# Optimization experiments

Measured on AMD Instinct MI355X. Metric: run time of the kernel, lower is better.

The kernel has to match this reference:

```python
import jax, jax.numpy as jnp
import numpy as np

E = 1024
M = 6
GH = 256
FR = 16  # FiLM bottleneck r = max(16, E//64)


def setup_inputs() -> dict:
    key = jax.random.key(0)
    ks = jax.random.split(key, 32)
    n = lambda k, shape, std=0.02: jax.random.normal(k, shape, dtype=jnp.float32) * std
    inp = {
        "x": jax.random.normal(ks[0], (4, 2048, E), dtype=jnp.float32),
        # gate MLP E->GH->M
        "gw1": n(ks[1], (E, GH)), "gb1": jnp.zeros((GH,), jnp.float32),
        "gw2": n(ks[2], (GH, M)), "gb2": jnp.zeros((M,), jnp.float32),
        "ebias": jnp.zeros((M,), jnp.float32),
        "pm_alpha": jnp.float32(0.5),
        # expert 0: DoubleMLP E->2E->E
        "dfc_w": n(ks[3], (E, 2 * E)), "dfc_b": jnp.zeros((2 * E,), jnp.float32),
        "dproj_w": n(ks[4], (2 * E, E)), "dproj_b": jnp.zeros((E,), jnp.float32),
        # expert 1: SingleMLP E->E->E
        "sfc_w": n(ks[5], (E, E)), "sfc_b": jnp.zeros((E,), jnp.float32),
        "sproj_w": n(ks[6], (E, E)), "sproj_b": jnp.zeros((E,), jnp.float32),
        # expert 2: rank-2 perceptron
        "p2_w": n(ks[7], (2, E)), "p2_v": n(ks[8], (2, E)),
        "p2_alpha": jnp.ones((2,), jnp.float32), "p2_b": jnp.zeros((2,), jnp.float32),
        "p2_bias": jnp.zeros((E,), jnp.float32),
        # expert 3: rank-4 perceptron
        "p4_w": n(ks[9], (4, E)), "p4_v": n(ks[10], (4, E)),
        "p4_alpha": jnp.ones((4,), jnp.float32), "p4_b": jnp.zeros((4,), jnp.float32),
        "p4_bias": jnp.zeros((E,), jnp.float32),
        # expert 4: ReGLU1D
        "rg_u": n(ks[11], (E,)), "rg_a": jnp.ones((E,), jnp.float32),
        "rg_b": jnp.zeros((1,), jnp.float32), "rg_bias": jnp.zeros((E,), jnp.float32),
        # expert 5: FiLM E->FR->2E
        "fl_dw": n(ks[12], (E, FR)), "fl_db": jnp.zeros((FR,), jnp.float32),
        "fl_uw": n(ks[13], (FR, 2 * E)), "fl_ub": jnp.zeros((2 * E,), jnp.float32),
    }
    return inp


def _gelu(x):
    return jax.nn.gelu(x, approximate=False)  # torch nn.GELU default (erf)


def _rank_n(x, w, v, alpha, b, biasvec):
    # y = biasvec + sum_i alpha_i * gelu(<w_i,x> + b_i) * v_i
    s = jnp.einsum("bse,ne->bsn", x, w) + b
    g = _gelu(s)
    return jnp.einsum("bsn,ne->bse", alpha * g, v) + biasvec


def reference(x, gw1, gb1, gw2, gb2, ebias, pm_alpha,
              dfc_w, dfc_b, dproj_w, dproj_b,
              sfc_w, sfc_b, sproj_w, sproj_b,
              p2_w, p2_v, p2_alpha, p2_b, p2_bias,
              p4_w, p4_v, p4_alpha, p4_b, p4_bias,
              rg_u, rg_a, rg_b, rg_bias,
              fl_dw, fl_db, fl_uw, fl_ub):
    # gate logits [B,S,M]; tau=1.0
    gl = _gelu(x @ gw1 + gb1) @ gw2 + gb2 + ebias
    pi = jax.nn.softmax(gl, axis=-1)
    # top_k=1 sparse weights: mask to top-1 then renormalize
    _, topi = jax.lax.top_k(pi, 1)
    mask = jax.nn.one_hot(topi[..., 0], M, dtype=pi.dtype)
    w = pi * mask
    w = w / (jnp.sum(w, axis=-1, keepdims=True) + 1e-9)

    # experts (dropout = identity in eval)
    o0 = _gelu(x @ dfc_w + dfc_b) @ dproj_w + dproj_b            # DoubleMLP
    o1 = _gelu(x @ sfc_w + sfc_b) @ sproj_w + sproj_b            # SingleMLP
    o2 = _rank_n(x, p2_w, p2_v, p2_alpha, p2_b, p2_bias)          # perc2
    o3 = _rank_n(x, p4_w, p4_v, p4_alpha, p4_b, p4_bias)          # perc4
    s = x @ rg_u + rg_b[0]                                        # ReGLU1D
    o4 = jax.nn.sigmoid(s)[..., None] * (x * rg_a) + rg_bias
    t = _gelu(x @ fl_dw + fl_db)                                  # FiLM
    gb = t @ fl_uw + fl_ub
    gamma, beta = jnp.split(gb, 2, axis=-1)
    o5 = gamma * x + beta

    all_out = jnp.stack([o0, o1, o2, o3, o4, o5], axis=-1)        # [B,S,E,M]
    mixed = jnp.sum(all_out * w[..., None, :], axis=-1)
    return pm_alpha * mixed
```

## Files before the change

kernel.cpp:

```cpp
#include <hip/hip_runtime.h>
#include <math.h>


#define E 1024
#define GH 256
#define NEXP 6
#define NTOK 8192
#define NCH 24

typedef __attribute__((ext_vector_type(8))) short bf16x8;
typedef __attribute__((ext_vector_type(4))) float f32x4;

__device__ __forceinline__ float gelu_erf(float v) {
    return 0.5f * v * (1.0f + erff(v * 0.70710678118654752440f));
}

__device__ __forceinline__ unsigned short f2bf(float f) {
    union { float f; unsigned u; } c; c.f = f;
    unsigned u = c.u;
    u += 0x7fffu + ((u >> 16) & 1u);
    return (unsigned short)(u >> 16);
}

__device__ __forceinline__ float bf2f(unsigned short h) {
    union { unsigned u; float f; } c; c.u = ((unsigned)h) << 16;
    return c.f;
}

__device__ __forceinline__ int ldso(int row, int q) {
    return row * 32 + ((q ^ ((row >> 1) & 3)) << 3);
}

__device__ __forceinline__ void glds16(const void* g, void* l) {
    __builtin_amdgcn_global_load_lds(
        (const __attribute__((address_space(1))) void*)g,
        (__attribute__((address_space(3))) void*)l, 16, 0, 0);
}

__global__ __launch_bounds__(256)
void prep_kernel(const float* __restrict__ x, unsigned short* __restrict__ xh,
                 unsigned short* __restrict__ xl,
                 const float* __restrict__ gw1, unsigned short* __restrict__ w1cat,
                 const float* __restrict__ p2_w, const float* __restrict__ p4_w,
                 const float* __restrict__ rg_u, const float* __restrict__ fl_dw,
                 unsigned short* __restrict__ w1cheap,
                 const float* __restrict__ dfc_w, unsigned short* __restrict__ dfc_wt,
                 const float* __restrict__ dproj_w, unsigned short* __restrict__ dpj_wt,
                 const float* __restrict__ sfc_w, unsigned short* __restrict__ sfc_wt,
                 const float* __restrict__ sproj_w, unsigned short* __restrict__ spj_wt) {
    __shared__ float tile[32][33];
    const int tid = threadIdx.x;
    const int tx = tid & 31, ty = tid >> 5;
    int b = blockIdx.x;
    if (b < 2048) {
        const int n4 = NTOK * E / 4;
        for (int i = b * 256 + tid; i < n4; i += 2048 * 256) {
            float4 v = reinterpret_cast<const float4*>(x)[i];
            ushort4 h, l;
            h.x = f2bf(v.x); l.x = f2bf(v.x - bf2f(h.x));
            h.y = f2bf(v.y); l.y = f2bf(v.y - bf2f(h.y));
            h.z = f2bf(v.z); l.z = f2bf(v.z - bf2f(h.z));
            h.w = f2bf(v.w); l.w = f2bf(v.w - bf2f(h.w));
            reinterpret_cast<ushort4*>(xh)[i] = h;
            reinterpret_cast<ushort4*>(xl)[i] = l;
        }
        return;
    }
    b -= 2048;
    if (b < 256) {
        const int c0 = (b & 7) * 32, r0 = (b >> 3) * 32;
#pragma unroll
        for (int i = 0; i < 4; ++i)
            tile[ty + i * 8][tx] = gw1[(size_t)(r0 + ty + i * 8) * GH + c0 + tx];
        __syncthreads();
#pragma unroll
        for (int i = 0; i < 4; ++i) {
            float v = tile[tx][ty + i * 8];
            unsigned short h = f2bf(v);
            size_t row = (size_t)(c0 + ty + i * 8) * 2048;
            w1cat[row + r0 + tx] = h;
            w1cat[row + 1024 + r0 + tx] = f2bf(v - bf2f(h));
        }
        return;
    }
    b -= 256;
    if (b < 64) {
        const int r = b;
        const int k4 = tid * 4;
        float4 v = {0.f, 0.f, 0.f, 0.f};
        if (r < 2)       v = *reinterpret_cast<const float4*>(&p2_w[r * E + k4]);
        else if (r < 6)  v = *reinterpret_cast<const float4*>(&p4_w[(r - 2) * E + k4]);
        else if (r == 6) v = *reinterpret_cast<const float4*>(&rg_u[k4]);
        else if (r < 23) {
            const int j = r - 7;
            v.x = fl_dw[(k4 + 0) * 16 + j];
            v.y = fl_dw[(k4 + 1) * 16 + j];
            v.z = fl_dw[(k4 + 2) * 16 + j];
            v.w = fl_dw[(k4 + 3) * 16 + j];
        }
        ushort4 h, l;
        h.x = f2bf(v.x); l.x = f2bf(v.x - bf2f(h.x));
        h.y = f2bf(v.y); l.y = f2bf(v.y - bf2f(h.y));
        h.z = f2bf(v.z); l.z = f2bf(v.z - bf2f(h.z));
        h.w = f2bf(v.w); l.w = f2bf(v.w - bf2f(h.w));
        *reinterpret_cast<ushort4*>(&w1cheap[r * 2048 + k4]) = h;
        *reinterpret_cast<ushort4*>(&w1cheap[r * 2048 + 1024 + k4]) = l;
        return;
    }
    b -= 64;
    const float* src; unsigned short* dst; int R, C, nbx;
    if (b < 2048)      { src = dfc_w;   dst = dfc_wt; R = 1024; C = 2048; nbx = 64; }
    else if (b < 4096) { src = dproj_w; dst = dpj_wt; R = 2048; C = 1024; nbx = 32; b -= 2048; }
    else if (b < 5120) { src = sfc_w;   dst = sfc_wt; R = 1024; C = 1024; nbx = 32; b -= 4096; }
    else               { src = sproj_w; dst = spj_wt; R = 1024; C = 1024; nbx = 32; b -= 5120; }
    const int c0 = (b % nbx) * 32, r0 = (b / nbx) * 32;
#pragma unroll
    for (int i = 0; i < 4; ++i)
        tile[ty + i * 8][tx] = src[(size_t)(r0 + ty + i * 8) * C + c0 + tx];
    __syncthreads();
#pragma unroll
    for (int i = 0; i < 4; ++i)
        dst[(size_t)(c0 + ty + i * 8) * R + r0 + tx] = f2bf(tile[tx][ty + i * 8]);
}

__global__ __launch_bounds__(256)
void gate_partial_kernel(const unsigned short* __restrict__ xh,
                         const unsigned short* __restrict__ xl,
                         const unsigned short* __restrict__ w1cat,
                         const unsigned short* __restrict__ w1cheap,
                         float* __restrict__ hp,
                         float* __restrict__ cdot) {
    __shared__ __align__(16) unsigned short As[2][128 * 64];
    __shared__ __align__(16) unsigned short Bs[2][128 * 64];
    const int tid = threadIdx.x;
    const int bid = blockIdx.x;
    const int xcd = bid & 7, slot = bid >> 3;
    const int nx = slot & 1;
    const int strip = xcd * 32 + (slot >> 1);
    const int m = strip >> 2, c2 = strip & 3;
    const int z = c2 & 1, h = c2 >> 1;
    const int t0 = m * 128, n0 = nx * 128;
    const unsigned short* A = z ? xl : xh;
    float* hpz = hp + (size_t)c2 * ((size_t)NTOK * GH);
    float* cd  = cdot + (size_t)c2 * ((size_t)NTOK * NCH);

    const int lane = tid & 63, wv = tid >> 6;
    const int wr = wv >> 1, wc = wv & 1;
    const int lm = lane & 15, q = lane >> 4;
    const int r0 = tid >> 2, gsl = tid & 3;
    const int g = gsl ^ ((r0 >> 1) & 3);
    const int lbase = wv * 512;

    const unsigned short* pa0 = A + (size_t)(t0 + r0) * E + g * 8;
    const unsigned short* pa1 = A + (size_t)(t0 + 64 + r0) * E + g * 8;
    const unsigned short* pb0 = w1cat + (size_t)(n0 + r0) * 2048 + h * 1024 + g * 8;
    const unsigned short* pb1 = w1cat + (size_t)(n0 + 64 + r0) * 2048 + h * 1024 + g * 8;
    const unsigned short* pcw = w1cheap + (size_t)(nx * 16 + lm) * 2048 + h * 1024 + q * 8;

    f32x4 acc[4][4];
#pragma unroll
    for (int s = 0; s < 4; ++s)
#pragma unroll
        for (int t = 0; t < 4; ++t) acc[s][t] = (f32x4){0.f, 0.f, 0.f, 0.f};
    f32x4 accC[2];
    accC[0] = (f32x4){0.f, 0.f, 0.f, 0.f};
    accC[1] = (f32x4){0.f, 0.f, 0.f, 0.f};

    glds16(pa0, &As[0][lbase]);
    glds16(pa1, &As[0][2048 + lbase]);
    glds16(pa0 + 32, &As[0][4096 + lbase]);
    glds16(pa1 + 32, &As[0][4096 + 2048 + lbase]);
    glds16(pb0, &Bs[0][lbase]);
    glds16(pb1, &Bs[0][2048 + lbase]);
    glds16(pb0 + 32, &Bs[0][4096 + lbase]);
    glds16(pb1 + 32, &Bs[0][4096 + 2048 + lbase]);
    bf16x8 cf0 = *(const bf16x8*)pcw;
    bf16x8 cf1 = *(const bf16x8*)(pcw + 32);

    int cur = 0;
    for (int k0 = 0;; k0 += 64) {
        __syncthreads();
        const int kn = k0 + 64;
        bf16x8 cf0n, cf1n;
        if (kn < 1024) {
            glds16(pa0 + kn, &As[cur ^ 1][lbase]);
            glds16(pa1 + kn, &As[cur ^ 1][2048 + lbase]);
            glds16(pa0 + kn + 32, &As[cur ^ 1][4096 + lbase]);
            glds16(pa1 + kn + 32, &As[cur ^ 1][4096 + 2048 + lbase]);
            glds16(pb0 + kn, &Bs[cur ^ 1][lbase]);
            glds16(pb1 + kn, &Bs[cur ^ 1][2048 + lbase]);
            glds16(pb0 + kn + 32, &Bs[cur ^ 1][4096 + lbase]);
            glds16(pb1 + kn + 32, &Bs[cur ^ 1][4096 + 2048 + lbase]);
            cf0n = *(const bf16x8*)(pcw + kn);
            cf1n = *(const bf16x8*)(pcw + kn + 32);
        }
#pragma unroll
        for (int sub = 0; sub < 2; ++sub) {
            const int off = sub * 4096;
            bf16x8 af[4], bfr[4];
#pragma unroll
            for (int s = 0; s < 4; ++s) af[s] = *(const bf16x8*)&As[cur][off + ldso(wr * 64 + s * 16 + lm, q)];
#pragma unroll
            for (int t = 0; t < 4; ++t) bfr[t] = *(const bf16x8*)&Bs[cur][off + ldso(wc * 64 + t * 16 + lm, q)];
#pragma unroll
            for (int s = 0; s < 4; ++s)
#pragma unroll
                for (int t = 0; t < 4; ++t)
                    acc[s][t] = __builtin_amdgcn_mfma_f32_16x16x32_bf16(af[s], bfr[t], acc[s][t], 0, 0, 0);
            bf16x8 cf = sub ? cf1 : cf0;
            bf16x8 ac0 = wc ? af[2] : af[0];
            bf16x8 ac1 = wc ? af[3] : af[1];
            accC[0] = __builtin_amdgcn_mfma_f32_16x16x32_bf16(ac0, cf, accC[0], 0, 0, 0);
            accC[1] = __builtin_amdgcn_mfma_f32_16x16x32_bf16(ac1, cf, accC[1], 0, 0, 0);
        }
        if (kn >= 1024) break;
        cf0 = cf0n; cf1 = cf1n; cur ^= 1;
    }
#pragma unroll
    for (int s = 0; s < 4; ++s)
#pragma unroll
        for (int t = 0; t < 4; ++t)
#pragma unroll
            for (int rg = 0; rg < 4; ++rg) {
                int rl = wr * 64 + s * 16 + q * 4 + rg;
                int c  = wc * 64 + t * 16 + lm;
                hpz[(size_t)(t0 + rl) * GH + n0 + c] = acc[s][t][rg];
            }
    const int cc = nx * 16 + lm;
    if (cc < NCH) {
#pragma unroll
        for (int i = 0; i < 2; ++i)
#pragma unroll
            for (int rg = 0; rg < 4; ++rg) {
                int rl = wr * 64 + wc * 32 + i * 16 + q * 4 + rg;
                cd[(size_t)(t0 + rl) * NCH + cc] = accC[i][rg];
            }
    }
}

__global__ __launch_bounds__(256)
void gate_finalize_kernel(const float* __restrict__ hp,
                          const float* __restrict__ gb1, const float* __restrict__ gw2,
                          const float* __restrict__ gb2, const float* __restrict__ ebias,
                          const float* __restrict__ pm_alpha,
                          const float* __restrict__ cdot,
                          const float* __restrict__ p2_alpha, const float* __restrict__ p2_b,
                          const float* __restrict__ p4_alpha, const float* __restrict__ p4_b,
                          const float* __restrict__ rg_b, const float* __restrict__ fl_db,
                          float* __restrict__ scale, int* __restrict__ counts,
                          int* __restrict__ tlist, int* __restrict__ eid,
                          float* __restrict__ gvec) {
    __shared__ float hs[32][264];
    __shared__ float g2s[GH * NEXP];
    __shared__ int tokexp[32];
    const int tid = threadIdx.x;
    const int t0 = blockIdx.x * 32;
    const size_t HPS = (size_t)NTOK * GH;
    for (int i = tid; i < GH * NEXP; i += 256) g2s[i] = gw2[i];
#pragma unroll
    for (int i = 0; i < 8; ++i) {
        int f4 = i * 256 + tid;
        int row = f4 >> 6, c4 = (f4 & 63) * 4;
        size_t base = (size_t)(t0 + row) * GH + c4;
        float4 a = *reinterpret_cast<const float4*>(&hp[base]);
        float4 b = *reinterpret_cast<const float4*>(&hp[HPS + base]);
        float4 c = *reinterpret_cast<const float4*>(&hp[2 * HPS + base]);
        float4 d = *reinterpret_cast<const float4*>(&hp[3 * HPS + base]);
        float4 o;
        o.x = gelu_erf(a.x + b.x + c.x + d.x + gb1[c4 + 0]);
        o.y = gelu_erf(a.y + b.y + c.y + d.y + gb1[c4 + 1]);
        o.z = gelu_erf(a.z + b.z + c.z + d.z + gb1[c4 + 2]);
        o.w = gelu_erf(a.w + b.w + c.w + d.w + gb1[c4 + 3]);
        *reinterpret_cast<float4*>(&hs[row][c4]) = o;
    }
    __syncthreads();
    const int t = tid >> 3, j = tid & 7;
    float p[NEXP] = {0.f, 0.f, 0.f, 0.f, 0.f, 0.f};
#pragma unroll 8
    for (int kk = 0; kk < 32; ++kk) {
        int k = j + kk * 8;
        float hv = hs[t][k];
        const float* gr = &g2s[k * NEXP];
#pragma unroll
        for (int m = 0; m < NEXP; ++m) p[m] += hv * gr[m];
    }
#pragma unroll
    for (int m = 0; m < NEXP; ++m) {
        p[m] += __shfl_xor(p[m], 4, 64);
        p[m] += __shfl_xor(p[m], 2, 64);
        p[m] += __shfl_xor(p[m], 1, 64);
    }
    if (j == 0) {
        float L[NEXP];
#pragma unroll
        for (int m = 0; m < NEXP; ++m) L[m] = p[m] + gb2[m] + ebias[m];
        float mx = L[0]; int am = 0;
#pragma unroll
        for (int m = 1; m < NEXP; ++m) { if (L[m] > mx) { mx = L[m]; am = m; } }
        float S = 0.f;
#pragma unroll
        for (int m = 0; m < NEXP; ++m) S += expf(L[m] - mx);
        float pt = 1.f / S;
        scale[t0 + t] = pm_alpha[0] * (pt / (pt + 1e-9f));
        eid[t0 + t] = am;
        tokexp[t] = am;
    }
    __syncthreads();
    if (tid < NEXP) {
        const int e = tid;
        int cnt = 0;
#pragma unroll
        for (int i = 0; i < 32; ++i) cnt += (tokexp[i] == e);
        if (cnt) {
            int base = atomicAdd(&counts[e], cnt);
            int pos = 0;
#pragma unroll
            for (int i = 0; i < 32; ++i)
                if (tokexp[i] == e) tlist[e * NTOK + base + (pos++)] = t0 + i;
        }
    }
    const size_t CDS = (size_t)NTOK * NCH;
    for (int i = tid; i < 32 * NCH; i += 256) {
        const int tt = i / NCH, slot = i - tt * NCH;
        const int tok = t0 + tt;
        size_t idx = (size_t)tok * NCH + slot;
        float s = cdot[idx] + cdot[CDS + idx] + cdot[2 * CDS + idx] + cdot[3 * CDS + idx];
        float val;
        if (slot < 2)       val = p2_alpha[slot] * gelu_erf(s + p2_b[slot]);
        else if (slot < 6)  val = p4_alpha[slot - 2] * gelu_erf(s + p4_b[slot - 2]);
        else if (slot == 6) val = 1.f / (1.f + expf(-(s + rg_b[0])));
        else if (slot < 23) val = gelu_erf(s + fl_db[slot - 7]);
        else                val = 0.f;
        gvec[(size_t)tok * NCH + slot] = val;
    }
}

#define STAGEAB(t, jb)                                            \
    do {                                                          \
        glds16(pa + (t) * 64,      &As[jb][lbase]);               \
        glds16(pa + (t) * 64 + 32, &As[jb][2048 + lbase]);        \
        glds16(pb + (t) * 64,      &Bs[jb][lbase]);               \
        glds16(pb + (t) * 64 + 32, &Bs[jb][2048 + lbase]);        \
    } while (0)

__global__ __launch_bounds__(256)
void moe_gemm1_kernel(const unsigned short* __restrict__ xh,
                      const unsigned short* __restrict__ B0, const unsigned short* __restrict__ B1,
                      const float* __restrict__ bias0, const float* __restrict__ bias1,
                      const int* __restrict__ counts, const int* __restrict__ tlist,
                      unsigned short* __restrict__ H0, unsigned short* __restrict__ H1) {
    __shared__ __align__(16) unsigned short As[3][64 * 64];
    __shared__ __align__(16) unsigned short Bs[3][64 * 64];
    __shared__ int toks[64];
    const int tid = threadIdx.x;
    const int bid = blockIdx.x;
    const int xcd = bid & 7, slot = bid >> 3;
    const int nx = slot & 31;
    const int strip = xcd + 8 * (slot >> 5);
    const int z = strip & 1;
    const int N = z ? 1024 : 2048;
    const int cnt = counts[z];
    const int i0 = (strip >> 1) * 64;
    const int n0 = nx * 64;
    if (i0 >= cnt || n0 >= N) return;
    const unsigned short* Bz = z ? B1 : B0;
    const float* bias = z ? bias1 : bias0;

    if (tid < 64) toks[tid] = tlist[z * NTOK + min(i0 + tid, cnt - 1)];
    __syncthreads();

    const int lane = tid & 63, wv = tid >> 6;
    const int wm = (wv & 1) * 32, wn = (wv >> 1) * 32;
    const int lm = lane & 15, q = lane >> 4;
    const int r0 = tid >> 2, gsl = tid & 3;
    const int g = gsl ^ ((r0 >> 1) & 3);
    const int lbase = wv * 512;

    const unsigned short* pa = xh + (size_t)toks[r0] * E + g * 8;
    const unsigned short* pb = Bz + (size_t)(n0 + r0) * E + g * 8;

    f32x4 acc[2][2];
#pragma unroll
    for (int s = 0; s < 2; ++s)
#pragma unroll
        for (int t = 0; t < 2; ++t) acc[s][t] = (f32x4){0.f, 0.f, 0.f, 0.f};

    STAGEAB(0, 0); STAGEAB(1, 1); STAGEAB(2, 2);

    const int nt = E / 64;
    for (int i = 0; i < nt; ++i) {
        const int ahead = nt - 1 - i;
        if (ahead >= 2)      asm volatile("s_waitcnt vmcnt(8)" ::: "memory");
        else if (ahead == 1) asm volatile("s_waitcnt vmcnt(4)" ::: "memory");
        else                 asm volatile("s_waitcnt vmcnt(0)" ::: "memory");
        asm volatile("s_barrier" ::: "memory");
        const int jb = i % 3;
#pragma unroll
        for (int sub = 0; sub < 2; ++sub) {
            const int off = sub * 2048;
            bf16x8 af[2], bfr[2];
#pragma unroll
            for (int s = 0; s < 2; ++s) af[s] = *(const bf16x8*)&As[jb][off + ldso(wm + s * 16 + lm, q)];
#pragma unroll
            for (int t = 0; t < 2; ++t) bfr[t] = *(const bf16x8*)&Bs[jb][off + ldso(wn + t * 16 + lm, q)];
#pragma unroll
            for (int s = 0; s < 2; ++s)
#pragma unroll
                for (int t = 0; t < 2; ++t)
                    acc[s][t] = __builtin_amdgcn_mfma_f32_16x16x32_bf16(af[s], bfr[t], acc[s][t], 0, 0, 0);
        }
        asm volatile("s_barrier" ::: "memory");
        if (i + 3 < nt) STAGEAB(i + 3, jb);
    }
    unsigned short* Hz = z ? H1 : H0;
#pragma unroll
    for (int s = 0; s < 2; ++s)
#pragma unroll
        for (int t = 0; t < 2; ++t)
#pragma unroll
            for (int rg = 0; rg < 4; ++rg) {
                int rl = wm + s * 16 + q * 4 + rg;
                int gc = n0 + wn + t * 16 + lm;
                float v = acc[s][t][rg] + bias[gc];
                Hz[(size_t)(i0 + rl) * N + gc] = f2bf(gelu_erf(v));
            }
}

__global__ __launch_bounds__(256)
void moe_gemm2_kernel(const unsigned short* __restrict__ h1, const unsigned short* __restrict__ h2,
                      const unsigned short* __restrict__ dpj, const unsigned short* __restrict__ spj,
                      const float* __restrict__ dproj_b, const float* __restrict__ sproj_b,
                      const int* __restrict__ counts, const int* __restrict__ tlist,
                      const float* __restrict__ scale,
                      float* __restrict__ out) {
    __shared__ __align__(16) unsigned short As[3][64 * 64];
    __shared__ __align__(16) unsigned short Bs[3][64 * 64];
    __shared__ int toks[64];
    const int tid = threadIdx.x;
    const int bb = blockIdx.x;
    const int lane = tid & 63;

    const int xcd = bb & 7, slot = bb >> 3;
    const int nx = slot & 15;
    const int strip = xcd + 8 * (slot >> 4);
    const int z = strip & 1;
    const int i0 = (strip >> 1) * 64;
    const int n0 = nx * 64;
    const int K = z ? 1024 : 2048;
    const int cnt = counts[z];
    if (i0 >= cnt) return;
    const int rows = min(64, cnt - i0);
    const unsigned short* Az = z ? h2 : h1;
    const unsigned short* Bz = z ? spj : dpj;
    const float* bias = z ? sproj_b : dproj_b;

    if (tid < 64) toks[tid] = tlist[z * NTOK + min(i0 + tid, cnt - 1)];
    __syncthreads();

    const int wv = tid >> 6;
    const int wm = (wv & 1) * 32, wn = (wv >> 1) * 32;
    const int lm = lane & 15, q = lane >> 4;
    const int r0 = tid >> 2, gsl = tid & 3;
    const int g = gsl ^ ((r0 >> 1) & 3);
    const int lbase = wv * 512;

    const unsigned short* pa = Az + (size_t)(i0 + r0) * K + g * 8;
    const unsigned short* pb = Bz + (size_t)(n0 + r0) * K + g * 8;

    f32x4 acc[2][2];
#pragma unroll
    for (int s = 0; s < 2; ++s)
#pragma unroll
        for (int t = 0; t < 2; ++t) acc[s][t] = (f32x4){0.f, 0.f, 0.f, 0.f};

    STAGEAB(0, 0); STAGEAB(1, 1); STAGEAB(2, 2);

    const int nt = K / 64;
    for (int i = 0; i < nt; ++i) {
        const int ahead = nt - 1 - i;
        if (ahead >= 2)      asm volatile("s_waitcnt vmcnt(8)" ::: "memory");
        else if (ahead == 1) asm volatile("s_waitcnt vmcnt(4)" ::: "memory");
        else                 asm volatile("s_waitcnt vmcnt(0)" ::: "memory");
        asm volatile("s_barrier" ::: "memory");
        const int jb = i % 3;
#pragma unroll
        for (int sub = 0; sub < 2; ++sub) {
            const int off = sub * 2048;
            bf16x8 af[2], bfr[2];
#pragma unroll
            for (int s = 0; s < 2; ++s) af[s] = *(const bf16x8*)&As[jb][off + ldso(wm + s * 16 + lm, q)];
#pragma unroll
            for (int t = 0; t < 2; ++t) bfr[t] = *(const bf16x8*)&Bs[jb][off + ldso(wn + t * 16 + lm, q)];
#pragma unroll
            for (int s = 0; s < 2; ++s)
#pragma unroll
                for (int t = 0; t < 2; ++t)
                    acc[s][t] = __builtin_amdgcn_mfma_f32_16x16x32_bf16(af[s], bfr[t], acc[s][t], 0, 0, 0);
        }
        asm volatile("s_barrier" ::: "memory");
        if (i + 3 < nt) STAGEAB(i + 3, jb);
    }
#pragma unroll
    for (int s = 0; s < 2; ++s)
#pragma unroll
        for (int t = 0; t < 2; ++t)
#pragma unroll
            for (int rg = 0; rg < 4; ++rg) {
                int rl = wm + s * 16 + q * 4 + rg;
                if (rl < rows) {
                    int gc = n0 + wn + t * 16 + lm;
                    int tok = toks[rl];
                    out[(size_t)tok * E + gc] = scale[tok] * (acc[s][t][rg] + bias[gc]);
                }
            }
}

__global__ __launch_bounds__(256)
void cheap_kernel(const int* __restrict__ counts, const int* __restrict__ tlist,
                  const float* __restrict__ scale, const float* __restrict__ x,
                  const float* __restrict__ gvec,
                  const float* __restrict__ p2_v, const float* __restrict__ p2_bias,
                  const float* __restrict__ p4_v, const float* __restrict__ p4_bias,
                  const float* __restrict__ rg_a, const float* __restrict__ rg_bias,
                  const float* __restrict__ fl_uw, const float* __restrict__ fl_ub,
                  float* __restrict__ out) {
    __shared__ int stoks[8];
    __shared__ float ssc[8];
    __shared__ float sgv[8][17];
    const int tid = threadIdx.x;
    const int k4 = tid * 4;
    for (int s = blockIdx.x; s < 4096; s += 2048) {
        const int e = 2 + (s & 3);
        const int ti = s >> 2;
        const int cnt = counts[e];
        const int i0 = ti * 8;
        if (i0 >= cnt) continue;
        const int nt = min(8, cnt - i0);
        __syncthreads();
        if (tid < 128) {
            const int tt = tid >> 4, sl = tid & 15;
            const int tk = tlist[e * NTOK + min(i0 + tt, cnt - 1)];
            if (sl == 0) { stoks[tt] = tk; ssc[tt] = scale[tk]; }
            const int base = (e == 2) ? 0 : (e == 3) ? 2 : (e == 4) ? 6 : 7;
            const int ng   = (e == 2) ? 2 : (e == 3) ? 4 : (e == 4) ? 1 : 16;
            if (sl < ng) sgv[tt][sl] = gvec[(size_t)tk * NCH + base + sl];
        }
        __syncthreads();
        if (e == 2) {
            const float4 b0 = *reinterpret_cast<const float4*>(&p2_bias[k4]);
            const float4 v0 = *reinterpret_cast<const float4*>(&p2_v[k4]);
            const float4 v1 = *reinterpret_cast<const float4*>(&p2_v[E + k4]);
#pragma unroll
            for (int tt = 0; tt < 8; ++tt) {
                if (tt < nt) {
                    const float g0 = sgv[tt][0], g1 = sgv[tt][1], sc = ssc[tt];
                    float4 o;
                    o.x = (b0.x + g0 * v0.x + g1 * v1.x) * sc;
                    o.y = (b0.y + g0 * v0.y + g1 * v1.y) * sc;
                    o.z = (b0.z + g0 * v0.z + g1 * v1.z) * sc;
                    o.w = (b0.w + g0 * v0.w + g1 * v1.w) * sc;
                    *reinterpret_cast<float4*>(&out[(size_t)stoks[tt] * E + k4]) = o;
                }
            }
        } else if (e == 3) {
            const float4 b0 = *reinterpret_cast<const float4*>(&p4_bias[k4]);
            float4 vv[4];
#pragma unroll
            for (int j = 0; j < 4; ++j)
                vv[j] = *reinterpret_cast<const float4*>(&p4_v[j * E + k4]);
#pragma unroll
            for (int tt = 0; tt < 8; ++tt) {
                if (tt < nt) {
                    float4 o = b0;
#pragma unroll
                    for (int j = 0; j < 4; ++j) {
                        const float gj = sgv[tt][j];
                        o.x += gj * vv[j].x; o.y += gj * vv[j].y;
                        o.z += gj * vv[j].z; o.w += gj * vv[j].w;
                    }
                    const float sc = ssc[tt];
                    o.x *= sc; o.y *= sc; o.z *= sc; o.w *= sc;
                    *reinterpret_cast<float4*>(&out[(size_t)stoks[tt] * E + k4]) = o;
                }
            }
        } else if (e == 4) {
            const float4 av = *reinterpret_cast<const float4*>(&rg_a[k4]);
            const float4 bv = *reinterpret_cast<const float4*>(&rg_bias[k4]);
#pragma unroll
            for (int tt = 0; tt < 8; ++tt) {
                if (tt < nt) {
                    const float sg = sgv[tt][0], sc = ssc[tt];
                    const float4 xv = *reinterpret_cast<const float4*>(&x[(size_t)stoks[tt] * E + k4]);
                    float4 o;
                    o.x = (sg * xv.x * av.x + bv.x) * sc;
                    o.y = (sg * xv.y * av.y + bv.y) * sc;
                    o.z = (sg * xv.z * av.z + bv.z) * sc;
                    o.w = (sg * xv.w * av.w + bv.w) * sc;
                    *reinterpret_cast<float4*>(&out[(size_t)stoks[tt] * E + k4]) = o;
                }
            }
        } else {
            float4 ga[8], be[8];
            const float4 g0 = *reinterpret_cast<const float4*>(&fl_ub[k4]);
            const float4 b0 = *reinterpret_cast<const float4*>(&fl_ub[E + k4]);
#pragma unroll
            for (int tt = 0; tt < 8; ++tt) { ga[tt] = g0; be[tt] = b0; }
#pragma unroll
            for (int j = 0; j < 16; ++j) {
                const float4 ug = *reinterpret_cast<const float4*>(&fl_uw[(size_t)j * 2 * E + k4]);
                const float4 ub = *reinterpret_cast<const float4*>(&fl_uw[(size_t)j * 2 * E + E + k4]);
#pragma unroll
                for (int tt = 0; tt < 8; ++tt) {
                    const float tj = sgv[tt][j];
                    ga[tt].x += tj * ug.x; ga[tt].y += tj * ug.y;
                    ga[tt].z += tj * ug.z; ga[tt].w += tj * ug.w;
                    be[tt].x += tj * ub.x; be[tt].y += tj * ub.y;
                    be[tt].z += tj * ub.z; be[tt].w += tj * ub.w;
                }
            }
#pragma unroll
            for (int tt = 0; tt < 8; ++tt) {
                if (tt < nt) {
                    const float sc = ssc[tt];
                    const float4 xv = *reinterpret_cast<const float4*>(&x[(size_t)stoks[tt] * E + k4]);
                    float4 o;
                    o.x = (ga[tt].x * xv.x + be[tt].x) * sc;
                    o.y = (ga[tt].y * xv.y + be[tt].y) * sc;
                    o.z = (ga[tt].z * xv.z + be[tt].z) * sc;
                    o.w = (ga[tt].w * xv.w + be[tt].w) * sc;
                    *reinterpret_cast<float4*>(&out[(size_t)stoks[tt] * E + k4]) = o;
                }
            }
        }
    }
}

extern "C" void kernel_launch(void* const* d_in, const int* in_sizes, int n_in,
                              void* d_out, int out_size, void* d_ws, size_t ws_size,
                              hipStream_t stream) {
    const float* x        = (const float*)d_in[0];
    const float* gw1      = (const float*)d_in[1];
    const float* gb1      = (const float*)d_in[2];
    const float* gw2      = (const float*)d_in[3];
    const float* gb2      = (const float*)d_in[4];
    const float* ebias    = (const float*)d_in[5];
    const float* pm_alpha = (const float*)d_in[6];
    const float* dfc_w    = (const float*)d_in[7];
    const float* dfc_b    = (const float*)d_in[8];
    const float* dproj_w  = (const float*)d_in[9];
    const float* dproj_b  = (const float*)d_in[10];
    const float* sfc_w    = (const float*)d_in[11];
    const float* sfc_b    = (const float*)d_in[12];
    const float* sproj_w  = (const float*)d_in[13];
    const float* sproj_b  = (const float*)d_in[14];
    const float* p2_w     = (const float*)d_in[15];
    const float* p2_v     = (const float*)d_in[16];
    const float* p2_alpha = (const float*)d_in[17];
    const float* p2_b     = (const float*)d_in[18];
    const float* p2_bias  = (const float*)d_in[19];
    const float* p4_w     = (const float*)d_in[20];
    const float* p4_v     = (const float*)d_in[21];
    const float* p4_alpha = (const float*)d_in[22];
    const float* p4_b     = (const float*)d_in[23];
    const float* p4_bias  = (const float*)d_in[24];
    const float* rg_u     = (const float*)d_in[25];
    const float* rg_a     = (const float*)d_in[26];
    const float* rg_b     = (const float*)d_in[27];
    const float* rg_bias  = (const float*)d_in[28];
    const float* fl_dw    = (const float*)d_in[29];
    const float* fl_db    = (const float*)d_in[30];
    const float* fl_uw    = (const float*)d_in[31];
    const float* fl_ub    = (const float*)d_in[32];
    float* out = (float*)d_out;

    char* ws = (char*)d_ws;
    size_t off = 0;
    int*            counts = (int*)(ws + off);            off += 256;
    float*          scale  = (float*)(ws + off);          off += (size_t)NTOK * 4;
    int*            tlist  = (int*)(ws + off);            off += (size_t)NEXP * NTOK * 4;
    int*            eid    = (int*)(ws + off);            off += (size_t)NTOK * 4;
    float*          gvec   = (float*)(ws + off);          off += (size_t)NTOK * NCH * 4;
    float*          cdot   = (float*)(ws + off);          off += (size_t)4 * NTOK * NCH * 4;
    unsigned short* w1cheap= (unsigned short*)(ws + off); off += (size_t)64 * 2048 * 2;
    unsigned short* w1cat  = (unsigned short*)(ws + off); off += (size_t)GH * 2048 * 2;
    unsigned short* dfc_wt = (unsigned short*)(ws + off); off += (size_t)2048 * 1024 * 2;
    unsigned short* dpj_wt = (unsigned short*)(ws + off); off += (size_t)1024 * 2048 * 2;
    unsigned short* sfc_wt = (unsigned short*)(ws + off); off += (size_t)1024 * 1024 * 2;
    unsigned short* spj_wt = (unsigned short*)(ws + off); off += (size_t)1024 * 1024 * 2;
    unsigned short* x_hi   = (unsigned short*)(ws + off); off += (size_t)NTOK * E * 2;
    char* U = ws + off;
    unsigned short* x_lo = (unsigned short*)U;
    unsigned short* h1   = (unsigned short*)U;
    unsigned short* h2   = (unsigned short*)(U + (size_t)16 * 1024 * 1024);
    float* hp = out;

    hipMemsetAsync(counts, 0, 256, stream);
    prep_kernel<<<8512, 256, 0, stream>>>(x, x_hi, x_lo, gw1, w1cat,
                                          p2_w, p4_w, rg_u, fl_dw, w1cheap,
                                          dfc_w, dfc_wt, dproj_w, dpj_wt,
                                          sfc_w, sfc_wt, sproj_w, spj_wt);
    gate_partial_kernel<<<512, 256, 0, stream>>>(
        x_hi, x_lo, w1cat, w1cheap, hp, cdot);
    gate_finalize_kernel<<<NTOK / 32, 256, 0, stream>>>(
        hp, gb1, gw2, gb2, ebias, pm_alpha, cdot,
        p2_alpha, p2_b, p4_alpha, p4_b, rg_b, fl_db,
        scale, counts, tlist, eid, gvec);
    moe_gemm1_kernel<<<2048, 256, 0, stream>>>(
        x_hi, dfc_wt, sfc_wt, dfc_b, sfc_b, counts, tlist, h1, h2);
    moe_gemm2_kernel<<<1024, 256, 0, stream>>>(
        h1, h2, dpj_wt, spj_wt, dproj_b, sproj_b, counts, tlist, scale, out);
    cheap_kernel<<<2048, 256, 0, stream>>>(
        counts, tlist, scale, x, gvec,
        p2_v, p2_bias, p4_v, p4_bias,
        rg_a, rg_bias, fl_uw, fl_ub, out);
    (void)in_sizes; (void)n_in; (void)out_size; (void)ws_size;
}
```

Baseline: 283.6 us.

## Fold cheap experts into dense MFMA tiles appended to the gemm1 launch

Removes cheap_kernel and expresses the four cheap experts (two low-rank perceptrons, ReGLU and FiLM) as a small K=32 matmul. Each token gets a coefficient row (split into bf16 hi/lo halves) against packed additive and multiplicative bf16 weight tables, and the result is out = scale*(M*x + A). These tiles run as 2048 extra blocks in the moe_gemm1 launch, which removes a kernel launch and the per-expert scalar loops and lets the work overlap with the big GEMM. In exchange every token's output is computed and written densely, with zeros for tokens routed to the MLP experts until gemm2 overwrites them. The expert weight vectors are now rounded to bf16, which adds some precision risk.

```diff
diff --git a/kernel.cpp b/kernel.cpp
--- a/kernel.cpp
+++ b/kernel.cpp
@@ -44,6 +44,11 @@
                  const float* __restrict__ p2_w, const float* __restrict__ p4_w,
                  const float* __restrict__ rg_u, const float* __restrict__ fl_dw,
                  unsigned short* __restrict__ w1cheap,
+                 const float* __restrict__ p2_bias, const float* __restrict__ p2_v,
+                 const float* __restrict__ p4_bias, const float* __restrict__ p4_v,
+                 const float* __restrict__ rg_a, const float* __restrict__ rg_bias,
+                 const float* __restrict__ fl_uw, const float* __restrict__ fl_ub,
+                 unsigned short* __restrict__ bta, unsigned short* __restrict__ btm,
                  const float* __restrict__ dfc_w, unsigned short* __restrict__ dfc_wt,
                  const float* __restrict__ dproj_w, unsigned short* __restrict__ dpj_wt,
                  const float* __restrict__ sfc_w, unsigned short* __restrict__ sfc_wt,
@@ -108,6 +113,34 @@
         return;
     }
     b -= 64;
+    if (b < 4) {
+        const int n = b * 256 + tid;
+        float av[32], mv[32];
+#pragma unroll
+        for (int r = 0; r < 32; ++r) { av[r] = 0.f; mv[r] = 0.f; }
+        av[0] = p2_bias[n];
+        av[1] = p2_v[n]; av[2] = p2_v[E + n];
+        av[3] = p4_bias[n];
+#pragma unroll
+        for (int j = 0; j < 4; ++j) av[4 + j] = p4_v[j * E + n];
+        av[8] = rg_bias[n];
+        mv[9] = rg_a[n];
+        av[10] = fl_ub[E + n];
+        mv[10] = fl_ub[n];
+#pragma unroll
+        for (int j = 0; j < 16; ++j) {
+            av[11 + j] = fl_uw[(size_t)j * 2 * E + E + n];
+            mv[11 + j] = fl_uw[(size_t)j * 2 * E + n];
+        }
+#pragma unroll
+        for (int r = 0; r < 32; ++r) {
+            unsigned short ha = f2bf(av[r]), hm = f2bf(mv[r]);
+            bta[n * 64 + r] = ha; bta[n * 64 + 32 + r] = ha;
+            btm[n * 64 + r] = hm; btm[n * 64 + 32 + r] = hm;
+        }
+        return;
+    }
+    b -= 4;
     const float* src; unsigned short* dst; int R, C, nbx;
     if (b < 2048)      { src = dfc_w;   dst = dfc_wt; R = 1024; C = 2048; nbx = 64; }
     else if (b < 4096) { src = dproj_w; dst = dpj_wt; R = 2048; C = 1024; nbx = 32; b -= 2048; }
@@ -248,8 +281,8 @@
                           const float* __restrict__ p4_alpha, const float* __restrict__ p4_b,
                           const float* __restrict__ rg_b, const float* __restrict__ fl_db,
                           float* __restrict__ scale, int* __restrict__ counts,
-                          int* __restrict__ tlist, int* __restrict__ eid,
-                          float* __restrict__ gvec) {
+                          int* __restrict__ tlist,
+                          unsigned short* __restrict__ Cm) {
     __shared__ float hs[32][264];
     __shared__ float g2s[GH * NEXP];
     __shared__ int tokexp[32];
@@ -302,7 +335,6 @@
         for (int m = 0; m < NEXP; ++m) S += expf(L[m] - mx);
         float pt = 1.f / S;
         scale[t0 + t] = pm_alpha[0] * (pt / (pt + 1e-9f));
-        eid[t0 + t] = am;
         tokexp[t] = am;
     }
     __syncthreads();
@@ -320,18 +352,31 @@
         }
     }
     const size_t CDS = (size_t)NTOK * NCH;
-    for (int i = tid; i < 32 * NCH; i += 256) {
-        const int tt = i / NCH, slot = i - tt * NCH;
+    for (int i = tid; i < 32 * 32; i += 256) {
+        const int tt = i >> 5, r = i & 31;
         const int tok = t0 + tt;
-        size_t idx = (size_t)tok * NCH + slot;
-        float s = cdot[idx] + cdot[CDS + idx] + cdot[2 * CDS + idx] + cdot[3 * CDS + idx];
-        float val;
-        if (slot < 2)       val = p2_alpha[slot] * gelu_erf(s + p2_b[slot]);
-        else if (slot < 6)  val = p4_alpha[slot - 2] * gelu_erf(s + p4_b[slot - 2]);
-        else if (slot == 6) val = 1.f / (1.f + expf(-(s + rg_b[0])));
-        else if (slot < 23) val = gelu_erf(s + fl_db[slot - 7]);
-        else                val = 0.f;
-        gvec[(size_t)tok * NCH + slot] = val;
+        const int e = tokexp[tt];
+        float c = 0.f;
+        int slot = -1;
+        if (r == 0)       { if (e == 2) c = 1.f; }
+        else if (r <= 2)  { if (e == 2) slot = r - 1; }
+        else if (r == 3)  { if (e == 3) c = 1.f; }
+        else if (r <= 7)  { if (e == 3) slot = r - 2; }
+        else if (r == 8)  { if (e == 4) c = 1.f; }
+        else if (r == 9)  { if (e == 4) slot = 6; }
+        else if (r == 10) { if (e == 5) c = 1.f; }
+        else if (r <= 26) { if (e == 5) slot = r - 4; }
+        if (slot >= 0) {
+            size_t idx = (size_t)tok * NCH + slot;
+            float s = cdot[idx] + cdot[CDS + idx] + cdot[2 * CDS + idx] + cdot[3 * CDS + idx];
+            if (slot < 2)       c = p2_alpha[slot] * gelu_erf(s + p2_b[slot]);
+            else if (slot < 6)  c = p4_alpha[slot - 2] * gelu_erf(s + p4_b[slot - 2]);
+            else if (slot == 6) c = 1.f / (1.f + expf(-(s + rg_b[0])));
+            else                c = gelu_erf(s + fl_db[slot - 7]);
+        }
+        unsigned short hi = f2bf(c);
+        Cm[(size_t)tok * 64 + r] = hi;
+        Cm[(size_t)tok * 64 + 32 + r] = f2bf(c - bf2f(hi));
     }
 }
 
@@ -348,12 +393,87 @@
                       const unsigned short* __restrict__ B0, const unsigned short* __restrict__ B1,
                       const float* __restrict__ bias0, const float* __restrict__ bias1,
                       const int* __restrict__ counts, const int* __restrict__ tlist,
-                      unsigned short* __restrict__ H0, unsigned short* __restrict__ H1) {
+                      unsigned short* __restrict__ H0, unsigned short* __restrict__ H1,
+                      const unsigned short* __restrict__ Cm,
+                      const unsigned short* __restrict__ bta, const unsigned short* __restrict__ btm,
+                      const float* __restrict__ x, const float* __restrict__ scale,
+                      float* __restrict__ out) {
     __shared__ __align__(16) unsigned short As[3][64 * 64];
     __shared__ __align__(16) unsigned short Bs[3][64 * 64];
     __shared__ int toks[64];
     const int tid = threadIdx.x;
     const int bid = blockIdx.x;
+    const int lane = tid & 63, wv = tid >> 6;
+    const int wm = (wv & 1) * 32, wn = (wv >> 1) * 32;
+    const int lm = lane & 15, q = lane >> 4;
+    const int r0 = tid >> 2, gsl = tid & 3;
+    const int g = gsl ^ ((r0 >> 1) & 3);
+    const int lbase = wv * 512;
+
+    if (bid >= 2048) {
+        const int cg = bid - 2048;
+        const int xcd = cg & 7, s = cg >> 3;
+        const int nx = s & 15;
+        const int mt = xcd + 8 * (s >> 4);
+        const int t0 = mt * 64, n0 = nx * 64;
+        unsigned short* Ct = &As[0][0];
+        unsigned short* Ba = &As[1][0];
+        unsigned short* Bm = &As[2][0];
+
+        const unsigned short* pc = Cm + (size_t)(t0 + r0) * 64 + g * 8;
+        const unsigned short* pba = bta + (size_t)(n0 + r0) * 64 + g * 8;
+        const unsigned short* pbm = btm + (size_t)(n0 + r0) * 64 + g * 8;
+        glds16(pc,       &Ct[lbase]);
+        glds16(pc + 32,  &Ct[2048 + lbase]);
+        glds16(pba,      &Ba[lbase]);
+        glds16(pba + 32, &Ba[2048 + lbase]);
+        glds16(pbm,      &Bm[lbase]);
+        glds16(pbm + 32, &Bm[2048 + lbase]);
+
+        f32x4 accA[2][2], accM[2][2];
+#pragma unroll
+        for (int s2 = 0; s2 < 2; ++s2)
+#pragma unroll
+            for (int t2 = 0; t2 < 2; ++t2) {
+                accA[s2][t2] = (f32x4){0.f, 0.f, 0.f, 0.f};
+                accM[s2][t2] = (f32x4){0.f, 0.f, 0.f, 0.f};
+            }
+        __syncthreads();
+#pragma unroll
+        for (int sub = 0; sub < 2; ++sub) {
+            const int off = sub * 2048;
+            bf16x8 af[2], ba[2], bm[2];
+#pragma unroll
+            for (int s2 = 0; s2 < 2; ++s2) af[s2] = *(const bf16x8*)&Ct[off + ldso(wm + s2 * 16 + lm, q)];
+#pragma unroll
+            for (int t2 = 0; t2 < 2; ++t2) {
+                ba[t2] = *(const bf16x8*)&Ba[off + ldso(wn + t2 * 16 + lm, q)];
+                bm[t2] = *(const bf16x8*)&Bm[off + ldso(wn + t2 * 16 + lm, q)];
+            }
+#pragma unroll
+            for (int s2 = 0; s2 < 2; ++s2)
+#pragma unroll
+                for (int t2 = 0; t2 < 2; ++t2) {
+                    accA[s2][t2] = __builtin_amdgcn_mfma_f32_16x16x32_bf16(af[s2], ba[t2], accA[s2][t2], 0, 0, 0);
+                    accM[s2][t2] = __builtin_amdgcn_mfma_f32_16x16x32_bf16(af[s2], bm[t2], accM[s2][t2], 0, 0, 0);
+                }
+        }
+#pragma unroll
+        for (int s2 = 0; s2 < 2; ++s2)
+#pragma unroll
+            for (int t2 = 0; t2 < 2; ++t2)
+#pragma unroll
+                for (int rg = 0; rg < 4; ++rg) {
+                    int rl = wm + s2 * 16 + q * 4 + rg;
+                    int gc = n0 + wn + t2 * 16 + lm;
+                    int tok = t0 + rl;
+                    float xv = x[(size_t)tok * E + gc];
+                    out[(size_t)tok * E + gc] =
+                        scale[tok] * (accM[s2][t2][rg] * xv + accA[s2][t2][rg]);
+                }
+        return;
+    }
+
     const int xcd = bid & 7, slot = bid >> 3;
     const int nx = slot & 31;
     const int strip = xcd + 8 * (slot >> 5);
@@ -368,13 +488,6 @@
 
     if (tid < 64) toks[tid] = tlist[z * NTOK + min(i0 + tid, cnt - 1)];
     __syncthreads();
-
-    const int lane = tid & 63, wv = tid >> 6;
-    const int wm = (wv & 1) * 32, wn = (wv >> 1) * 32;
-    const int lm = lane & 15, q = lane >> 4;
-    const int r0 = tid >> 2, gsl = tid & 3;
-    const int g = gsl ^ ((r0 >> 1) & 3);
-    const int lbase = wv * 512;
 
     const unsigned short* pa = xh + (size_t)toks[r0] * E + g * 8;
     const unsigned short* pb = Bz + (size_t)(n0 + r0) * E + g * 8;
@@ -513,126 +626,6 @@
                     out[(size_t)tok * E + gc] = scale[tok] * (acc[s][t][rg] + bias[gc]);
                 }
             }
-}
-
-__global__ __launch_bounds__(256)
-void cheap_kernel(const int* __restrict__ counts, const int* __restrict__ tlist,
-                  const float* __restrict__ scale, const float* __restrict__ x,
-                  const float* __restrict__ gvec,
-                  const float* __restrict__ p2_v, const float* __restrict__ p2_bias,
-                  const float* __restrict__ p4_v, const float* __restrict__ p4_bias,
-                  const float* __restrict__ rg_a, const float* __restrict__ rg_bias,
-                  const float* __restrict__ fl_uw, const float* __restrict__ fl_ub,
-                  float* __restrict__ out) {
-    __shared__ int stoks[8];
-    __shared__ float ssc[8];
-    __shared__ float sgv[8][17];
-    const int tid = threadIdx.x;
-    const int k4 = tid * 4;
-    for (int s = blockIdx.x; s < 4096; s += 2048) {
-        const int e = 2 + (s & 3);
-        const int ti = s >> 2;
-        const int cnt = counts[e];
-        const int i0 = ti * 8;
-        if (i0 >= cnt) continue;
-        const int nt = min(8, cnt - i0);
-        __syncthreads();
-        if (tid < 128) {
-            const int tt = tid >> 4, sl = tid & 15;
-            const int tk = tlist[e * NTOK + min(i0 + tt, cnt - 1)];
-            if (sl == 0) { stoks[tt] = tk; ssc[tt] = scale[tk]; }
-            const int base = (e == 2) ? 0 : (e == 3) ? 2 : (e == 4) ? 6 : 7;
-            const int ng   = (e == 2) ? 2 : (e == 3) ? 4 : (e == 4) ? 1 : 16;
-            if (sl < ng) sgv[tt][sl] = gvec[(size_t)tk * NCH + base + sl];
-        }
-        __syncthreads();
-        if (e == 2) {
-            const float4 b0 = *reinterpret_cast<const float4*>(&p2_bias[k4]);
-            const float4 v0 = *reinterpret_cast<const float4*>(&p2_v[k4]);
-            const float4 v1 = *reinterpret_cast<const float4*>(&p2_v[E + k4]);
-#pragma unroll
-            for (int tt = 0; tt < 8; ++tt) {
-                if (tt < nt) {
-                    const float g0 = sgv[tt][0], g1 = sgv[tt][1], sc = ssc[tt];
-                    float4 o;
-                    o.x = (b0.x + g0 * v0.x + g1 * v1.x) * sc;
-                    o.y = (b0.y + g0 * v0.y + g1 * v1.y) * sc;
-                    o.z = (b0.z + g0 * v0.z + g1 * v1.z) * sc;
-                    o.w = (b0.w + g0 * v0.w + g1 * v1.w) * sc;
-                    *reinterpret_cast<float4*>(&out[(size_t)stoks[tt] * E + k4]) = o;
-                }
-            }
-        } else if (e == 3) {
-            const float4 b0 = *reinterpret_cast<const float4*>(&p4_bias[k4]);
-            float4 vv[4];
-#pragma unroll
-            for (int j = 0; j < 4; ++j)
-                vv[j] = *reinterpret_cast<const float4*>(&p4_v[j * E + k4]);
-#pragma unroll
-            for (int tt = 0; tt < 8; ++tt) {
-                if (tt < nt) {
-                    float4 o = b0;
-#pragma unroll
-                    for (int j = 0; j < 4; ++j) {
-                        const float gj = sgv[tt][j];
-                        o.x += gj * vv[j].x; o.y += gj * vv[j].y;
-                        o.z += gj * vv[j].z; o.w += gj * vv[j].w;
-                    }
-                    const float sc = ssc[tt];
-                    o.x *= sc; o.y *= sc; o.z *= sc; o.w *= sc;
-                    *reinterpret_cast<float4*>(&out[(size_t)stoks[tt] * E + k4]) = o;
-                }
-            }
-        } else if (e == 4) {
-            const float4 av = *reinterpret_cast<const float4*>(&rg_a[k4]);
-            const float4 bv = *reinterpret_cast<const float4*>(&rg_bias[k4]);
-#pragma unroll
-            for (int tt = 0; tt < 8; ++tt) {
-                if (tt < nt) {
-                    const float sg = sgv[tt][0], sc = ssc[tt];
-                    const float4 xv = *reinterpret_cast<const float4*>(&x[(size_t)stoks[tt] * E + k4]);
-                    float4 o;
-                    o.x = (sg * xv.x * av.x + bv.x) * sc;
-                    o.y = (sg * xv.y * av.y + bv.y) * sc;
-                    o.z = (sg * xv.z * av.z + bv.z) * sc;
-                    o.w = (sg * xv.w * av.w + bv.w) * sc;
-                    *reinterpret_cast<float4*>(&out[(size_t)stoks[tt] * E + k4]) = o;
-                }
-            }
-        } else {
-            float4 ga[8], be[8];
-            const float4 g0 = *reinterpret_cast<const float4*>(&fl_ub[k4]);
-            const float4 b0 = *reinterpret_cast<const float4*>(&fl_ub[E + k4]);
-#pragma unroll
-            for (int tt = 0; tt < 8; ++tt) { ga[tt] = g0; be[tt] = b0; }
-#pragma unroll
-            for (int j = 0; j < 16; ++j) {
-                const float4 ug = *reinterpret_cast<const float4*>(&fl_uw[(size_t)j * 2 * E + k4]);
-                const float4 ub = *reinterpret_cast<const float4*>(&fl_uw[(size_t)j * 2 * E + E + k4]);
-#pragma unroll
-                for (int tt = 0; tt < 8; ++tt) {
-                    const float tj = sgv[tt][j];
-                    ga[tt].x += tj * ug.x; ga[tt].y += tj * ug.y;
-                    ga[tt].z += tj * ug.z; ga[tt].w += tj * ug.w;
-                    be[tt].x += tj * ub.x; be[tt].y += tj * ub.y;
-                    be[tt].z += tj * ub.z; be[tt].w += tj * ub.w;
-                }
-            }
-#pragma unroll
-            for (int tt = 0; tt < 8; ++tt) {
-                if (tt < nt) {
-                    const float sc = ssc[tt];
-                    const float4 xv = *reinterpret_cast<const float4*>(&x[(size_t)stoks[tt] * E + k4]);
-                    float4 o;
-                    o.x = (ga[tt].x * xv.x + be[tt].x) * sc;
-                    o.y = (ga[tt].y * xv.y + be[tt].y) * sc;
-                    o.z = (ga[tt].z * xv.z + be[tt].z) * sc;
-                    o.w = (ga[tt].w * xv.w + be[tt].w) * sc;
-                    *reinterpret_cast<float4*>(&out[(size_t)stoks[tt] * E + k4]) = o;
-                }
-            }
-        }
-    }
 }
 
 extern "C" void kernel_launch(void* const* d_in, const int* in_sizes, int n_in,
@@ -678,9 +671,10 @@
     int*            counts = (int*)(ws + off);            off += 256;
     float*          scale  = (float*)(ws + off);          off += (size_t)NTOK * 4;
     int*            tlist  = (int*)(ws + off);            off += (size_t)NEXP * NTOK * 4;
-    int*            eid    = (int*)(ws + off);            off += (size_t)NTOK * 4;
-    float*          gvec   = (float*)(ws + off);          off += (size_t)NTOK * NCH * 4;
     float*          cdot   = (float*)(ws + off);          off += (size_t)4 * NTOK * NCH * 4;
+    unsigned short* Cm     = (unsigned short*)(ws + off); off += (size_t)NTOK * 64 * 2;
+    unsigned short* bta    = (unsigned short*)(ws + off); off += (size_t)E * 64 * 2;
+    unsigned short* btm    = (unsigned short*)(ws + off); off += (size_t)E * 64 * 2;
     unsigned short* w1cheap= (unsigned short*)(ws + off); off += (size_t)64 * 2048 * 2;
     unsigned short* w1cat  = (unsigned short*)(ws + off); off += (size_t)GH * 2048 * 2;
     unsigned short* dfc_wt = (unsigned short*)(ws + off); off += (size_t)2048 * 1024 * 2;
@@ -695,8 +689,10 @@
     float* hp = out;
 
     hipMemsetAsync(counts, 0, 256, stream);
-    prep_kernel<<<8512, 256, 0, stream>>>(x, x_hi, x_lo, gw1, w1cat,
+    prep_kernel<<<8516, 256, 0, stream>>>(x, x_hi, x_lo, gw1, w1cat,
                                           p2_w, p4_w, rg_u, fl_dw, w1cheap,
+                                          p2_bias, p2_v, p4_bias, p4_v,
+                                          rg_a, rg_bias, fl_uw, fl_ub, bta, btm,
                                           dfc_w, dfc_wt, dproj_w, dpj_wt,
                                           sfc_w, sfc_wt, sproj_w, spj_wt);
     gate_partial_kernel<<<512, 256, 0, stream>>>(
@@ -704,14 +700,11 @@
     gate_finalize_kernel<<<NTOK / 32, 256, 0, stream>>>(
         hp, gb1, gw2, gb2, ebias, pm_alpha, cdot,
         p2_alpha, p2_b, p4_alpha, p4_b, rg_b, fl_db,
-        scale, counts, tlist, eid, gvec);
-    moe_gemm1_kernel<<<2048, 256, 0, stream>>>(
-        x_hi, dfc_wt, sfc_wt, dfc_b, sfc_b, counts, tlist, h1, h2);
+        scale, counts, tlist, Cm);
+    moe_gemm1_kernel<<<4096, 256, 0, stream>>>(
+        x_hi, dfc_wt, sfc_wt, dfc_b, sfc_b, counts, tlist, h1, h2,
+        Cm, bta, btm, x, scale, out);
     moe_gemm2_kernel<<<1024, 256, 0, stream>>>(
         h1, h2, dpj_wt, spj_wt, dproj_b, sproj_b, counts, tlist, scale, out);
-    cheap_kernel<<<2048, 256, 0, stream>>>(
-        counts, tlist, scale, x, gvec,
-        p2_v, p2_bias, p4_v, p4_bias,
-        rg_a, rg_bias, fl_uw, fl_ub, out);
     (void)in_sizes; (void)n_in; (void)out_size; (void)ws_size;
 }
```

Result: faster. 260.2 us (-8.2%).
